# Performance work log

Measured on AMD Instinct MI355X. Metric: run time of the kernel, lower is better.

Reference implementation:

```python
import jax, jax.numpy as jnp
import numpy as np

# FP8 E4M3 constants (per FP8Handler)
E4M3_MAX = 240.0          # max_normal
MANTISSA_SCALE = 8.0      # 2 ** mantissa_bits (3)
SCALE_EPS = 1e-10


def setup_inputs() -> dict:
    key = jax.random.key(0)
    k1, k2, k3 = jax.random.split(key, 3)
    B, S, D_IN, D_OUT = 4, 2048, 4096, 4096
    x = jax.random.normal(k1, (B, S, D_IN), dtype=jnp.float32)
    weight = jax.random.normal(k2, (D_OUT, D_IN), dtype=jnp.float32)
    bias = jax.random.normal(k3, (D_OUT,), dtype=jnp.float32)
    return {"x": x, "weight": weight, "bias": bias}


def _fp8_e4m3_quant_dequant(w, scale):
    # FP8Handler.quantize_tensor + _simulate_e4m3_precision
    s = jnp.clip(w / scale, -E4M3_MAX, E4M3_MAX)
    s = s.astype(jnp.float16).astype(jnp.float32)  # fp16 round-trip
    q = jnp.round(s * MANTISSA_SCALE) / MANTISSA_SCALE  # mantissa truncation
    q = jnp.clip(q, -E4M3_MAX, E4M3_MAX)
    return q * scale


def reference(x, weight, bias):
    # FP8Quantizer.compute_scale: per-tensor max-abs, margin=0, fresh history
    amax = jnp.max(jnp.abs(weight))
    scale = jnp.maximum(amax / E4M3_MAX, SCALE_EPS)
    qw = _fp8_e4m3_quant_dequant(weight, scale)  # [out, in]
    # F.linear(x, qw, bias): x [b, s, in] @ qw.T [in, out] + bias
    return jnp.einsum('bsi,oi->bso', x, qw) + bias
```

## Files before the change

kernel.cpp:

```cpp
#include <hip/hip_runtime.h>
#include <hip/hip_bf16.h>
#include <hip/hip_fp16.h>

#define E4M3_MAX 240.0f

typedef __attribute__((ext_vector_type(8))) __bf16 bf16x8;
typedef __attribute__((ext_vector_type(4))) float f32x4;
typedef unsigned short ushort_t;

__device__ __forceinline__ void gload_lds16(const void* g, void* l) {
  __builtin_amdgcn_global_load_lds(
      (const __attribute__((address_space(1))) void*)g,
      (__attribute__((address_space(3))) void*)l,
      16, 0, 0);
}

__global__ void amax_abs_kernel(const float* __restrict__ w, int n4,
                                unsigned* __restrict__ amax_bits) {
  float m = 0.0f;
  const float4* w4 = (const float4*)w;
  int stride = gridDim.x * blockDim.x;
  for (int i = blockIdx.x * blockDim.x + threadIdx.x; i < n4; i += stride) {
    float4 v = w4[i];
    m = fmaxf(m, fmaxf(fmaxf(fabsf(v.x), fabsf(v.y)),
                       fmaxf(fabsf(v.z), fabsf(v.w))));
  }
  for (int off = 32; off > 0; off >>= 1)
    m = fmaxf(m, __shfl_down(m, off, 64));
  __shared__ float smax[4];
  int l = threadIdx.x & 63, wv = threadIdx.x >> 6;
  if (l == 0) smax[wv] = m;
  __syncthreads();
  if (threadIdx.x == 0) {
    float bm = fmaxf(fmaxf(smax[0], smax[1]), fmaxf(smax[2], smax[3]));
    atomicMax(amax_bits, __float_as_uint(bm));
  }
}

__global__ void quant_weight_kernel(const float* __restrict__ w,
                                    const unsigned* __restrict__ amax_bits,
                                    ushort_t* __restrict__ qw, int n4) {
  float amax = __uint_as_float(*amax_bits);
  float scale = fmaxf(amax / E4M3_MAX, 1e-10f);
  const float4* w4 = (const float4*)w;
  ushort4* q4 = (ushort4*)qw;
  int stride = gridDim.x * blockDim.x;
  for (int i = blockIdx.x * blockDim.x + threadIdx.x; i < n4; i += stride) {
    float4 v = w4[i];
    float r[4] = {v.x, v.y, v.z, v.w};
    ushort_t o[4];
#pragma unroll
    for (int j = 0; j < 4; ++j) {
      float s = fminf(fmaxf(r[j] / scale, -E4M3_MAX), E4M3_MAX);
      s = __half2float(__float2half(s));
      float q = rintf(s * 8.0f) * 0.125f;
      q = fminf(fmaxf(q, -E4M3_MAX), E4M3_MAX);
      __hip_bfloat16 h = __float2bfloat16(q * scale);
      o[j] = *(ushort_t*)&h;
    }
    ushort4 ov = {o[0], o[1], o[2], o[3]};
    q4[i] = ov;
  }
}

__global__ void cvt_bf16_kernel(const float* __restrict__ x,
                                ushort_t* __restrict__ xb, int n4) {
  const float4* x4 = (const float4*)x;
  ushort4* o4 = (ushort4*)xb;
  int stride = gridDim.x * blockDim.x;
  for (int i = blockIdx.x * blockDim.x + threadIdx.x; i < n4; i += stride) {
    float4 v = x4[i];
    __hip_bfloat16 h0 = __float2bfloat16(v.x);
    __hip_bfloat16 h1 = __float2bfloat16(v.y);
    __hip_bfloat16 h2 = __float2bfloat16(v.z);
    __hip_bfloat16 h3 = __float2bfloat16(v.w);
    ushort4 o = {*(ushort_t*)&h0, *(ushort_t*)&h1,
                 *(ushort_t*)&h2, *(ushort_t*)&h3};
    o4[i] = o;
  }
}


#define BAR() do { asm volatile("" ::: "memory"); \
                   __builtin_amdgcn_s_barrier(); \
                   asm volatile("" ::: "memory"); } while (0)
#define LGKM0() asm volatile("s_waitcnt lgkmcnt(0)" ::: "memory")
#define VMC4() asm volatile("s_waitcnt vmcnt(4)" ::: "memory")
#define VMC0() asm volatile("s_waitcnt vmcnt(0)" ::: "memory")
#define NOVM() do {} while (0)

__global__ __launch_bounds__(512, 2) void gemm256_bal(
    const ushort_t* __restrict__ A, const ushort_t* __restrict__ Bt,
    const float* __restrict__ bias, float* __restrict__ C) {
  constexpr int K = 4096, N = 4096;
  __shared__ __align__(16) ushort_t As[2][2][8192];
  __shared__ __align__(16) ushort_t Bs[2][2][8192];

  const int tid = threadIdx.x;
  const int wid = tid >> 6, lane = tid & 63;
  const int wm = wid >> 2, wn = wid & 3;
  const int lk = lane >> 4, lr = lane & 15;

  int bid = blockIdx.x;
  int swz = (bid & 7) * 64 + (bid >> 3);
  int bm = swz >> 4, bn = swz & 15;

  const ushort_t* Ab = A + (size_t)bm * 256 * K;
  const ushort_t* Bb = Bt + (size_t)bn * 256 * K;

  int offG[2];
#pragma unroll
  for (int q = 0; q < 2; ++q) {
    int s = q * 512 + tid;
    int row = s >> 3;
    int c = (s & 7) ^ (row & 7);
    offG[q] = row * K + c * 8;
  }

#define STAGE_AH(buf, kt, h)                                               \
  do { _Pragma("unroll") for (int q = 0; q < 2; ++q)                       \
    gload_lds16(Ab + (size_t)(h) * 128 * K + (kt) * 64 + offG[q],          \
                &As[buf][h][(q * 512 + wid * 64) * 8]); } while (0)
#define STAGE_BH(buf, kt, h)                                               \
  do { _Pragma("unroll") for (int q = 0; q < 2; ++q)                       \
    gload_lds16(Bb + (size_t)(h) * 128 * K + (kt) * 64 + offG[q],          \
                &Bs[buf][h][(q * 512 + wid * 64) * 8]); } while (0)

  const int abase = lr * 64;
  const int bbase = (wn & 1) * 4096 + lr * 64;
  const int bhalf = wn >> 1;
  const int xk0 = ((lk) ^ (lr & 7)) * 8;
  const int xk1 = ((4 + lk) ^ (lr & 7)) * 8;

  bf16x8 afA[4], afB[4], bfK0[4], bfK1[4];
  f32x4 acc[8][4] = {};

#define RD_A4(dst, buf, fi0, xkv)                                          \
  do { _Pragma("unroll") for (int i = 0; i < 4; ++i)                       \
    dst[i] = *(const bf16x8*)&As[buf][wm][abase + ((fi0) + i) * 1024 + (xkv)]; } while (0)
#define RD_B4K(dst, buf, xkv)                                              \
  do { _Pragma("unroll") for (int j = 0; j < 4; ++j)                       \
    dst[j] = *(const bf16x8*)&Bs[buf][bhalf][bbase + j * 1024 + (xkv)]; } while (0)

#define MMA16(areg, breg, FI0)                                             \
  do { __builtin_amdgcn_s_setprio(1);                                      \
    _Pragma("unroll") for (int i = 0; i < 4; ++i)                          \
      _Pragma("unroll") for (int j = 0; j < 4; ++j)                        \
        acc[(FI0) + i][j] = __builtin_amdgcn_mfma_f32_16x16x32_bf16(       \
            areg[i], breg[j], acc[(FI0) + i][j], 0, 0, 0);                 \
    __builtin_amdgcn_s_setprio(0); } while (0)

#define ITER(t, SA1, SB2, SA2, SB3, VM4K, VM8K)                            \
  do {                                                                     \
    RD_B4K(bfK0, 0, xk0); RD_A4(afA, 0, 0, xk0);                           \
    if (SA1) STAGE_AH(1, (t) + 1, 0);                                      \
    BAR(); LGKM0(); MMA16(afA, bfK0, 0); BAR();                            \
    RD_B4K(bfK1, 0, xk1); RD_A4(afB, 0, 4, xk0);                           \
    if (SA1) STAGE_AH(1, (t) + 1, 1);                                      \
    BAR(); LGKM0(); MMA16(afB, bfK0, 4); BAR();                            \
    RD_A4(afA, 0, 0, xk1);                                                 \
    if (SB2) STAGE_BH(0, (t) + 2, 0);                                      \
    BAR(); LGKM0(); MMA16(afA, bfK1, 0); BAR();                            \
    RD_A4(afB, 0, 4, xk1);                                                 \
    if (SB2) STAGE_BH(0, (t) + 2, 1);                                      \
    BAR(); LGKM0(); MMA16(afB, bfK1, 4); VM4K; BAR();                      \
    RD_B4K(bfK0, 1, xk0); RD_A4(afA, 1, 0, xk0);                           \
    if (SA2) STAGE_AH(0, (t) + 2, 0);                                      \
    BAR(); LGKM0(); MMA16(afA, bfK0, 0); BAR();                            \
    RD_B4K(bfK1, 1, xk1); RD_A4(afB, 1, 4, xk0);                           \
    if (SA2) STAGE_AH(0, (t) + 2, 1);                                      \
    BAR(); LGKM0(); MMA16(afB, bfK0, 4); BAR();                            \
    RD_A4(afA, 1, 0, xk1);                                                 \
    if (SB3) STAGE_BH(1, (t) + 3, 0);                                      \
    BAR(); LGKM0(); MMA16(afA, bfK1, 0); BAR();                            \
    RD_A4(afB, 1, 4, xk1);                                                 \
    if (SB3) STAGE_BH(1, (t) + 3, 1);                                      \
    BAR(); LGKM0(); MMA16(afB, bfK1, 4); VM8K; BAR();                      \
  } while (0)

  STAGE_AH(0, 0, 0); STAGE_AH(0, 0, 1);
  STAGE_BH(0, 0, 0); STAGE_BH(0, 0, 1);
  STAGE_BH(1, 1, 0); STAGE_BH(1, 1, 1);
  VMC4();
  BAR();

  for (int t = 0; t < 62; t += 2)
    ITER(t, 1, 1, 1, 1, VMC4(), VMC4());

  ITER(62, 1, 0, 0, 0, VMC0(), NOVM());

  float* Cb = C + (size_t)(bm * 256 + wm * 128) * N + bn * 256 + wn * 64;
#pragma unroll
  for (int fj = 0; fj < 4; ++fj) {
    int n = fj * 16 + lr;
    float bv = bias[bn * 256 + wn * 64 + n];
#pragma unroll
    for (int fi = 0; fi < 8; ++fi) {
      int m0 = fi * 16 + lk * 4;
#pragma unroll
      for (int r = 0; r < 4; ++r)
        Cb[(size_t)(m0 + r) * N + n] = acc[fi][fj][r] + bv;
    }
  }
}

extern "C" void kernel_launch(void* const* d_in, const int* in_sizes, int n_in,
                              void* d_out, int out_size, void* d_ws, size_t ws_size,
                              hipStream_t stream) {
  const float* x = (const float*)d_in[0];
  const float* wt = (const float*)d_in[1];
  const float* bias = (const float*)d_in[2];
  float* out = (float*)d_out;

  const int DIN = 4096;
  const int NW = in_sizes[1];
  const int M = in_sizes[0] / DIN;

  char* ws = (char*)d_ws;
  unsigned* amax_bits = (unsigned*)ws;
  ushort_t* qw = (ushort_t*)(ws + 256);
  ushort_t* xb = (ushort_t*)(ws + 256 + (size_t)NW * 2);

  hipMemsetAsync(amax_bits, 0, 4, stream);
  hipLaunchKernelGGL(amax_abs_kernel, dim3(1024), dim3(256), 0, stream,
                     wt, NW / 4, amax_bits);
  hipLaunchKernelGGL(quant_weight_kernel, dim3(2048), dim3(256), 0, stream,
                     wt, amax_bits, qw, NW / 4);
  hipLaunchKernelGGL(cvt_bf16_kernel, dim3(2048), dim3(256), 0, stream,
                     x, xb, (M * DIN) / 4);

  hipLaunchKernelGGL(gemm256_bal, dim3(512), dim3(512), 0, stream,
                     xb, qw, bias, out);
}
```

Measured before the change: 384.9 us.

## Switch GEMM to 32x32x16 MFMA tiles with reordered LDS staging schedule

After: 340.8 us. 11.4% less time.

```diff
diff --git a/kernel.cpp b/kernel.cpp
--- a/kernel.cpp
+++ b/kernel.cpp
@@ -5,7 +5,7 @@
 #define E4M3_MAX 240.0f
 
 typedef __attribute__((ext_vector_type(8))) __bf16 bf16x8;
-typedef __attribute__((ext_vector_type(4))) float f32x4;
+typedef __attribute__((ext_vector_type(16))) float f32x16;
 typedef unsigned short ushort_t;
 
 __device__ __forceinline__ void gload_lds16(const void* g, void* l) {
@@ -85,11 +85,12 @@
                    __builtin_amdgcn_s_barrier(); \
                    asm volatile("" ::: "memory"); } while (0)
 #define LGKM0() asm volatile("s_waitcnt lgkmcnt(0)" ::: "memory")
+#define LGKM8() asm volatile("s_waitcnt lgkmcnt(8)" ::: "memory")
 #define VMC4() asm volatile("s_waitcnt vmcnt(4)" ::: "memory")
 #define VMC0() asm volatile("s_waitcnt vmcnt(0)" ::: "memory")
 #define NOVM() do {} while (0)
 
-__global__ __launch_bounds__(512, 2) void gemm256_bal(
+__global__ __launch_bounds__(512, 2) void gemm256_w32(
     const ushort_t* __restrict__ A, const ushort_t* __restrict__ Bt,
     const float* __restrict__ bias, float* __restrict__ C) {
   constexpr int K = 4096, N = 4096;
@@ -99,7 +100,7 @@
   const int tid = threadIdx.x;
   const int wid = tid >> 6, lane = tid & 63;
   const int wm = wid >> 2, wn = wid & 3;
-  const int lk = lane >> 4, lr = lane & 15;
+  const int l31 = lane & 31, lk2 = lane >> 5, l7 = lane & 7;
 
   int bid = blockIdx.x;
   int swz = (bid & 7) * 64 + (bid >> 3);
@@ -126,61 +127,62 @@
     gload_lds16(Bb + (size_t)(h) * 128 * K + (kt) * 64 + offG[q],          \
                 &Bs[buf][h][(q * 512 + wid * 64) * 8]); } while (0)
 
-  const int abase = lr * 64;
-  const int bbase = (wn & 1) * 4096 + lr * 64;
   const int bhalf = wn >> 1;
-  const int xk0 = ((lk) ^ (lr & 7)) * 8;
-  const int xk1 = ((4 + lk) ^ (lr & 7)) * 8;
-
-  bf16x8 afA[4], afB[4], bfK0[4], bfK1[4];
-  f32x4 acc[8][4] = {};
-
-#define RD_A4(dst, buf, fi0, xkv)                                          \
-  do { _Pragma("unroll") for (int i = 0; i < 4; ++i)                       \
-    dst[i] = *(const bf16x8*)&As[buf][wm][abase + ((fi0) + i) * 1024 + (xkv)]; } while (0)
-#define RD_B4K(dst, buf, xkv)                                              \
-  do { _Pragma("unroll") for (int j = 0; j < 4; ++j)                       \
-    dst[j] = *(const bf16x8*)&Bs[buf][bhalf][bbase + j * 1024 + (xkv)]; } while (0)
-
-#define MMA16(areg, breg, FI0)                                             \
+  const int brow0 = (wn & 1) * 64;
+  int xks[4];
+#pragma unroll
+  for (int ks = 0; ks < 4; ++ks) xks[ks] = ((ks * 2 + lk2) ^ l7) * 8;
+
+  bf16x8 af[4][4], bf[2][4];
+  f32x16 acc[4][2] = {};
+
+#define RD_A32(buf, rg)                                                    \
+  do { _Pragma("unroll") for (int ks = 0; ks < 4; ++ks)                    \
+    af[rg][ks] = *(const bf16x8*)                                          \
+        &As[buf][wm][((rg) * 32 + l31) * 64 + xks[ks]]; } while (0)
+#define RD_B32(buf)                                                        \
+  do { _Pragma("unroll") for (int cg = 0; cg < 2; ++cg)                    \
+    _Pragma("unroll") for (int ks = 0; ks < 4; ++ks)                       \
+      bf[cg][ks] = *(const bf16x8*)                                        \
+          &Bs[buf][bhalf][(brow0 + cg * 32 + l31) * 64 + xks[ks]]; } while (0)
+
+#define MMA8(rg)                                                           \
   do { __builtin_amdgcn_s_setprio(1);                                      \
-    _Pragma("unroll") for (int i = 0; i < 4; ++i)                          \
-      _Pragma("unroll") for (int j = 0; j < 4; ++j)                        \
-        acc[(FI0) + i][j] = __builtin_amdgcn_mfma_f32_16x16x32_bf16(       \
-            areg[i], breg[j], acc[(FI0) + i][j], 0, 0, 0);                 \
+    _Pragma("unroll") for (int ks = 0; ks < 4; ++ks) {                     \
+      acc[rg][0] = __builtin_amdgcn_mfma_f32_32x32x16_bf16(                \
+          af[rg][ks], bf[0][ks], acc[rg][0], 0, 0, 0);                     \
+      acc[rg][1] = __builtin_amdgcn_mfma_f32_32x32x16_bf16(                \
+          af[rg][ks], bf[1][ks], acc[rg][1], 0, 0, 0);                     \
+    }                                                                      \
     __builtin_amdgcn_s_setprio(0); } while (0)
 
-#define ITER(t, SA1, SB2, SA2, SB3, VM4K, VM8K)                            \
+#define ITER(t, SB1, SA2, SB2, SA3, VM4, VM8)                              \
   do {                                                                     \
-    RD_B4K(bfK0, 0, xk0); RD_A4(afA, 0, 0, xk0);                           \
-    if (SA1) STAGE_AH(1, (t) + 1, 0);                                      \
-    BAR(); LGKM0(); MMA16(afA, bfK0, 0); BAR();                            \
-    RD_B4K(bfK1, 0, xk1); RD_A4(afB, 0, 4, xk0);                           \
-    if (SA1) STAGE_AH(1, (t) + 1, 1);                                      \
-    BAR(); LGKM0(); MMA16(afB, bfK0, 4); BAR();                            \
-    RD_A4(afA, 0, 0, xk1);                                                 \
+    RD_B32(0); RD_A32(0, 0);                                               \
+    if (SB1) STAGE_BH(1, (t) + 1, 0);                                      \
+    LGKM8(); BAR(); LGKM0(); MMA8(0); BAR();                               \
+    RD_A32(0, 1); RD_A32(0, 2); RD_A32(0, 3);                              \
+    if (SB1) STAGE_BH(1, (t) + 1, 1);                                      \
+    LGKM8(); BAR(); LGKM0(); MMA8(1); BAR();                               \
+    if (SA2) STAGE_AH(0, (t) + 2, 0);                                      \
+    BAR(); MMA8(2); BAR();                                                 \
+    if (SA2) STAGE_AH(0, (t) + 2, 1);                                      \
+    BAR(); MMA8(3); VM4; BAR();                                            \
+    RD_B32(1); RD_A32(1, 0);                                               \
     if (SB2) STAGE_BH(0, (t) + 2, 0);                                      \
-    BAR(); LGKM0(); MMA16(afA, bfK1, 0); BAR();                            \
-    RD_A4(afB, 0, 4, xk1);                                                 \
+    LGKM8(); BAR(); LGKM0(); MMA8(0); BAR();                               \
+    RD_A32(1, 1); RD_A32(1, 2); RD_A32(1, 3);                              \
     if (SB2) STAGE_BH(0, (t) + 2, 1);                                      \
-    BAR(); LGKM0(); MMA16(afB, bfK1, 4); VM4K; BAR();                      \
-    RD_B4K(bfK0, 1, xk0); RD_A4(afA, 1, 0, xk0);                           \
-    if (SA2) STAGE_AH(0, (t) + 2, 0);                                      \
-    BAR(); LGKM0(); MMA16(afA, bfK0, 0); BAR();                            \
-    RD_B4K(bfK1, 1, xk1); RD_A4(afB, 1, 4, xk0);                           \
-    if (SA2) STAGE_AH(0, (t) + 2, 1);                                      \
-    BAR(); LGKM0(); MMA16(afB, bfK0, 4); BAR();                            \
-    RD_A4(afA, 1, 0, xk1);                                                 \
-    if (SB3) STAGE_BH(1, (t) + 3, 0);                                      \
-    BAR(); LGKM0(); MMA16(afA, bfK1, 0); BAR();                            \
-    RD_A4(afB, 1, 4, xk1);                                                 \
-    if (SB3) STAGE_BH(1, (t) + 3, 1);                                      \
-    BAR(); LGKM0(); MMA16(afB, bfK1, 4); VM8K; BAR();                      \
+    LGKM8(); BAR(); LGKM0(); MMA8(1); BAR();                               \
+    if (SA3) STAGE_AH(1, (t) + 3, 0);                                      \
+    BAR(); MMA8(2); BAR();                                                 \
+    if (SA3) STAGE_AH(1, (t) + 3, 1);                                      \
+    BAR(); MMA8(3); VM8; BAR();                                            \
   } while (0)
 
   STAGE_AH(0, 0, 0); STAGE_AH(0, 0, 1);
   STAGE_BH(0, 0, 0); STAGE_BH(0, 0, 1);
-  STAGE_BH(1, 1, 0); STAGE_BH(1, 1, 1);
+  STAGE_AH(1, 1, 0); STAGE_AH(1, 1, 1);
   VMC4();
   BAR();
 
@@ -191,15 +193,16 @@
 
   float* Cb = C + (size_t)(bm * 256 + wm * 128) * N + bn * 256 + wn * 64;
 #pragma unroll
-  for (int fj = 0; fj < 4; ++fj) {
-    int n = fj * 16 + lr;
+  for (int cg = 0; cg < 2; ++cg) {
+    int n = cg * 32 + l31;
     float bv = bias[bn * 256 + wn * 64 + n];
 #pragma unroll
-    for (int fi = 0; fi < 8; ++fi) {
-      int m0 = fi * 16 + lk * 4;
-#pragma unroll
-      for (int r = 0; r < 4; ++r)
-        Cb[(size_t)(m0 + r) * N + n] = acc[fi][fj][r] + bv;
+    for (int rg = 0; rg < 4; ++rg) {
+#pragma unroll
+      for (int r = 0; r < 16; ++r) {
+        int row = rg * 32 + (r & 3) + 8 * (r >> 2) + 4 * lk2;
+        Cb[(size_t)row * N + n] = acc[rg][cg][r] + bv;
+      }
     }
   }
 }
@@ -229,6 +232,6 @@
   hipLaunchKernelGGL(cvt_bf16_kernel, dim3(2048), dim3(256), 0, stream,
                      x, xb, (M * DIN) / 4);
 
-  hipLaunchKernelGGL(gemm256_bal, dim3(512), dim3(512), 0, stream,
+  hipLaunchKernelGGL(gemm256_w32, dim3(512), dim3(512), 0, stream,
                      xb, qw, bias, out);
 }
```

## Restructure GEMM main loop into quadrant MMA phases with reordered LDS staging

Applied to the files above, without the earlier changes.

Measured after the change: 351.3 us. -8.7%, faster.

```diff
diff --git a/kernel.cpp b/kernel.cpp
--- a/kernel.cpp
+++ b/kernel.cpp
@@ -85,11 +85,13 @@
                    __builtin_amdgcn_s_barrier(); \
                    asm volatile("" ::: "memory"); } while (0)
 #define LGKM0() asm volatile("s_waitcnt lgkmcnt(0)" ::: "memory")
-#define VMC4() asm volatile("s_waitcnt vmcnt(4)" ::: "memory")
+#define LGKM8() asm volatile("s_waitcnt lgkmcnt(8)" ::: "memory")
+#define VMC6() asm volatile("s_waitcnt vmcnt(6)" ::: "memory")
+#define VMC8() asm volatile("s_waitcnt vmcnt(8)" ::: "memory")
 #define VMC0() asm volatile("s_waitcnt vmcnt(0)" ::: "memory")
 #define NOVM() do {} while (0)
 
-__global__ __launch_bounds__(512, 2) void gemm256_bal(
+__global__ __launch_bounds__(512, 2) void gemm256_q(
     const ushort_t* __restrict__ A, const ushort_t* __restrict__ Bt,
     const float* __restrict__ bias, float* __restrict__ C) {
   constexpr int K = 4096, N = 4096;
@@ -132,62 +134,74 @@
   const int xk0 = ((lk) ^ (lr & 7)) * 8;
   const int xk1 = ((4 + lk) ^ (lr & 7)) * 8;
 
-  bf16x8 afA[4], afB[4], bfK0[4], bfK1[4];
+  bf16x8 afE[4][2], afO[4][2], bfP[2][2], bfQ[2][2];
   f32x4 acc[8][4] = {};
 
-#define RD_A4(dst, buf, fi0, xkv)                                          \
-  do { _Pragma("unroll") for (int i = 0; i < 4; ++i)                       \
-    dst[i] = *(const bf16x8*)&As[buf][wm][abase + ((fi0) + i) * 1024 + (xkv)]; } while (0)
-#define RD_B4K(dst, buf, xkv)                                              \
-  do { _Pragma("unroll") for (int j = 0; j < 4; ++j)                       \
-    dst[j] = *(const bf16x8*)&Bs[buf][bhalf][bbase + j * 1024 + (xkv)]; } while (0)
-
-#define MMA16(areg, breg, FI0)                                             \
+#define RDA(AF, fi0, cb)                                                   \
+  do { _Pragma("unroll") for (int i = 0; i < 4; ++i) {                     \
+    AF[i][0] = *(const bf16x8*)&As[cb][wm][abase + ((fi0) + i) * 1024 + xk0]; \
+    AF[i][1] = *(const bf16x8*)&As[cb][wm][abase + ((fi0) + i) * 1024 + xk1]; \
+  } } while (0)
+#define RDB(BF, fj0, cb)                                                   \
+  do { _Pragma("unroll") for (int j = 0; j < 2; ++j) {                     \
+    BF[j][0] = *(const bf16x8*)&Bs[cb][bhalf][bbase + ((fj0) + j) * 1024 + xk0]; \
+    BF[j][1] = *(const bf16x8*)&Bs[cb][bhalf][bbase + ((fj0) + j) * 1024 + xk1]; \
+  } } while (0)
+
+#define MMAQ(AF, fi0, BF, fj0)                                             \
   do { __builtin_amdgcn_s_setprio(1);                                      \
     _Pragma("unroll") for (int i = 0; i < 4; ++i)                          \
-      _Pragma("unroll") for (int j = 0; j < 4; ++j)                        \
-        acc[(FI0) + i][j] = __builtin_amdgcn_mfma_f32_16x16x32_bf16(       \
-            areg[i], breg[j], acc[(FI0) + i][j], 0, 0, 0);                 \
+      _Pragma("unroll") for (int j = 0; j < 2; ++j) {                      \
+        acc[(fi0) + i][(fj0) + j] = __builtin_amdgcn_mfma_f32_16x16x32_bf16( \
+            AF[i][0], BF[j][0], acc[(fi0) + i][(fj0) + j], 0, 0, 0);       \
+        acc[(fi0) + i][(fj0) + j] = __builtin_amdgcn_mfma_f32_16x16x32_bf16( \
+            AF[i][1], BF[j][1], acc[(fi0) + i][(fj0) + j], 0, 0, 0);       \
+      }                                                                    \
     __builtin_amdgcn_s_setprio(0); } while (0)
 
-#define ITER(t, SA1, SB2, SA2, SB3, VM4K, VM8K)                            \
+#define BODY(u, S1, S3, S45, S78, VM4, VM8)                                \
   do {                                                                     \
-    RD_B4K(bfK0, 0, xk0); RD_A4(afA, 0, 0, xk0);                           \
-    if (SA1) STAGE_AH(1, (t) + 1, 0);                                      \
-    BAR(); LGKM0(); MMA16(afA, bfK0, 0); BAR();                            \
-    RD_B4K(bfK1, 0, xk1); RD_A4(afB, 0, 4, xk0);                           \
-    if (SA1) STAGE_AH(1, (t) + 1, 1);                                      \
-    BAR(); LGKM0(); MMA16(afB, bfK0, 4); BAR();                            \
-    RD_A4(afA, 0, 0, xk1);                                                 \
-    if (SB2) STAGE_BH(0, (t) + 2, 0);                                      \
-    BAR(); LGKM0(); MMA16(afA, bfK1, 0); BAR();                            \
-    RD_A4(afB, 0, 4, xk1);                                                 \
-    if (SB2) STAGE_BH(0, (t) + 2, 1);                                      \
-    BAR(); LGKM0(); MMA16(afB, bfK1, 4); VM4K; BAR();                      \
-    RD_B4K(bfK0, 1, xk0); RD_A4(afA, 1, 0, xk0);                           \
-    if (SA2) STAGE_AH(0, (t) + 2, 0);                                      \
-    BAR(); LGKM0(); MMA16(afA, bfK0, 0); BAR();                            \
-    RD_B4K(bfK1, 1, xk1); RD_A4(afB, 1, 4, xk0);                           \
-    if (SA2) STAGE_AH(0, (t) + 2, 1);                                      \
-    BAR(); LGKM0(); MMA16(afB, bfK0, 4); BAR();                            \
-    RD_A4(afA, 1, 0, xk1);                                                 \
-    if (SB3) STAGE_BH(1, (t) + 3, 0);                                      \
-    BAR(); LGKM0(); MMA16(afA, bfK1, 0); BAR();                            \
-    RD_A4(afB, 1, 4, xk1);                                                 \
-    if (SB3) STAGE_BH(1, (t) + 3, 1);                                      \
-    BAR(); LGKM0(); MMA16(afB, bfK1, 4); VM8K; BAR();                      \
+                                                                  \
+    RDA(afE, 0, 0); RDB(bfP, 0, 0);                                        \
+    if (S1) STAGE_AH(1, (u) + 1, 1);                                       \
+    LGKM8(); BAR(); LGKM0(); MMAQ(afE, 0, bfP, 0); BAR();                  \
+                                                                  \
+    RDB(bfQ, 2, 0);                                                        \
+    BAR(); LGKM0(); MMAQ(afE, 0, bfQ, 2); BAR();                           \
+                                                                  \
+    RDA(afO, 4, 0);                                                        \
+    if (S3) STAGE_BH(0, (u) + 2, 0);                                       \
+    BAR(); LGKM0(); MMAQ(afO, 4, bfQ, 2); BAR();                           \
+                                                                  \
+    if (S45) { STAGE_BH(0, (u) + 2, 1); STAGE_AH(0, (u) + 2, 0); }         \
+    VM4; BAR(); MMAQ(afO, 4, bfP, 0); BAR();                               \
+                                                                  \
+    RDA(afE, 0, 1); RDB(bfP, 0, 1);                                        \
+    if (S45) STAGE_AH(0, (u) + 2, 1);                                      \
+    LGKM8(); BAR(); LGKM0(); MMAQ(afE, 0, bfP, 0); BAR();                  \
+                                                                  \
+    RDB(bfQ, 2, 1);                                                        \
+    BAR(); LGKM0(); MMAQ(afE, 0, bfQ, 2); BAR();                           \
+                                                                  \
+    RDA(afO, 4, 1);                                                        \
+    if (S78) STAGE_BH(1, (u) + 3, 0);                                      \
+    BAR(); LGKM0(); MMAQ(afO, 4, bfQ, 2); BAR();                           \
+                                                                  \
+    if (S78) { STAGE_BH(1, (u) + 3, 1); STAGE_AH(1, (u) + 3, 0); }         \
+    VM8; BAR(); MMAQ(afO, 4, bfP, 0); BAR();                               \
   } while (0)
 
+  STAGE_BH(0, 0, 0); STAGE_BH(0, 0, 1);
   STAGE_AH(0, 0, 0); STAGE_AH(0, 0, 1);
-  STAGE_BH(0, 0, 0); STAGE_BH(0, 0, 1);
   STAGE_BH(1, 1, 0); STAGE_BH(1, 1, 1);
-  VMC4();
+  STAGE_AH(1, 1, 0); STAGE_AH(1, 1, 1);
+  VMC8();
   BAR();
 
-  for (int t = 0; t < 62; t += 2)
-    ITER(t, 1, 1, 1, 1, VMC4(), VMC4());
-
-  ITER(62, 1, 0, 0, 0, VMC0(), NOVM());
+  BODY(0, 0, 1, 1, 1, VMC6(), VMC6());
+  for (int u = 2; u < 62; u += 2)
+    BODY(u, 1, 1, 1, 1, VMC6(), VMC6());
+  BODY(62, 1, 0, 0, 0, VMC0(), NOVM());
 
   float* Cb = C + (size_t)(bm * 256 + wm * 128) * N + bn * 256 + wn * 64;
 #pragma unroll
@@ -229,6 +243,6 @@
   hipLaunchKernelGGL(cvt_bf16_kernel, dim3(2048), dim3(256), 0, stream,
                      x, xb, (M * DIN) / 4);
 
-  hipLaunchKernelGGL(gemm256_bal, dim3(512), dim3(512), 0, stream,
+  hipLaunchKernelGGL(gemm256_q, dim3(512), dim3(512), 0, stream,
                      xb, qw, bias, out);
 }
```
